# Optimization experiments

Hardware: AMD Instinct MI355X
Metric: run time of the kernel (lower is better)

The kernel has to match this reference:

```python
import jax, jax.numpy as jnp
import numpy as np

N = 6144      # nodes
NFEAT = 512
NHID = 256
NHEADS = 4
DHEAD = NHID // NHEADS  # 64
NEMBED = 128
NEG_INF = -9e15
LRELU_ALPHA = 0.2


def setup_inputs() -> dict:
    key = jax.random.key(0)
    k = jax.random.split(key, 8)
    x = jax.random.normal(k[0], (N, NFEAT), dtype=jnp.float32)
    adj = (jax.random.uniform(k[1], (N, N)) < 0.01).astype(jnp.int32)
    # per-head GAT params, packed over heads
    W = jax.random.normal(k[2], (NHEADS, NFEAT, DHEAD), dtype=jnp.float32) * 0.05
    a_src = jax.random.normal(k[3], (NHEADS, DHEAD), dtype=jnp.float32) * 0.05
    a_dst = jax.random.normal(k[4], (NHEADS, DHEAD), dtype=jnp.float32) * 0.05
    # output linear (init.normal_ std=0.05 per reset_parameters)
    lin_w = jax.random.normal(k[5], (NEMBED, NHID), dtype=jnp.float32) * 0.05
    lin_b = jnp.zeros((NEMBED,), dtype=jnp.float32)
    return {"x": x, "adj": adj, "W": W, "a_src": a_src, "a_dst": a_dst,
            "lin_w": lin_w, "lin_b": lin_b}


def _gat_forward(x, adj, W, a_src, a_dst, lin_w, lin_b):
    # Wh: [H, N, D]
    Wh = jnp.einsum('nf,hfd->hnd', x, W)
    # attention logits e_ij = leakyrelu(a_src.Wh_i + a_dst.Wh_j): [H, N, N]
    s = jnp.einsum('hnd,hd->hn', Wh, a_src)   # source term per node
    t = jnp.einsum('hnd,hd->hn', Wh, a_dst)   # target term per node
    e = s[:, :, None] + t[:, None, :]
    e = jax.nn.leaky_relu(e, negative_slope=LRELU_ALPHA)
    # mask by adjacency, softmax over neighbors
    e = jnp.where(adj[None, :, :] > 0, e, NEG_INF)
    attn = jax.nn.softmax(e, axis=-1)
    # aggregate and per-head ELU (concat=True GAT layer)
    h = jnp.einsum('hnm,hmd->hnd', attn, Wh)
    h = jax.nn.elu(h)
    # concat heads -> [N, NHID]
    h = jnp.transpose(h, (1, 0, 2)).reshape(N, NHID)
    # dropout is identity in eval mode; linear + ELU
    out = jax.nn.elu(h @ lin_w.T + lin_b)
    return out


def reference(x, adj, W, a_src, a_dst, lin_w, lin_b):
    return _gat_forward(x, adj, W, a_src, a_dst, lin_w, lin_b)
```

## Files before the change

kernel.cpp:

```cpp
#include <hip/hip_runtime.h>
#include <hip/hip_bf16.h>
#include <math.h>

#define N_NODES 6144
#define NFEAT 512
#define NHID 256
#define NHEADS 4
#define DHEAD 64
#define NEMBED 128
#define LRELU_ALPHA 0.2f
#define MAXC 256
#define ASTRIDE 20

static __device__ __forceinline__ unsigned short f2bf(float f) {
    unsigned u = __float_as_uint(f);
    unsigned r = (u + 0x7FFFu + ((u >> 16) & 1u)) >> 16;
    return (unsigned short)r;
}
static __device__ __forceinline__ float bfLo(unsigned u) { return __uint_as_float(u << 16); }
static __device__ __forceinline__ float bfHi(unsigned u) { return __uint_as_float(u & 0xffff0000u); }

__global__ __launch_bounds__(256) void gemm_scan(const float* __restrict__ x,
                                                 const float* __restrict__ W,
                                                 const float* __restrict__ a_src,
                                                 const float* __restrict__ a_dst,
                                                 const int* __restrict__ adj,
                                                 unsigned short* __restrict__ Whb,
                                                 float* __restrict__ s_arr,
                                                 float* __restrict__ t_arr,
                                                 int* __restrict__ cnt_g,
                                                 unsigned short* __restrict__ nbr_g) {
    __shared__ float As[64][ASTRIDE];
    __shared__ float Bs[16][64];
    __shared__ int scnt;
    const int tid = threadIdx.x;

    if (blockIdx.y < NHEADS) {
        const int tx = tid & 15;
        const int ty = tid >> 4;
        const int row0 = blockIdx.x * 64;
        const int h = blockIdx.y;
        const float* Bp = W + (size_t)h * NFEAT * DHEAD;

        float acc[4][4] = {};

        for (int k0 = 0; k0 < NFEAT; k0 += 16) {
            {
                const int r = tid >> 2, kq = tid & 3;
                const float4 v = *(const float4*)(x + (size_t)(row0 + r) * NFEAT + k0 + kq * 4);
                *(float4*)&As[r][kq * 4] = v;
            }
            {
                const int kk = tid >> 4, cq = tid & 15;
                const float4 v = *(const float4*)(Bp + (size_t)(k0 + kk) * DHEAD + cq * 4);
                *(float4*)&Bs[kk][cq * 4] = v;
            }
            __syncthreads();
#pragma unroll
            for (int kk = 0; kk < 16; kk++) {
                float a[4], b[4];
#pragma unroll
                for (int i = 0; i < 4; i++) a[i] = As[ty * 4 + i][kk];
#pragma unroll
                for (int j = 0; j < 4; j++) b[j] = Bs[kk][tx * 4 + j];
#pragma unroll
                for (int i = 0; i < 4; i++)
#pragma unroll
                    for (int j = 0; j < 4; j++) acc[i][j] += a[i] * b[j];
            }
            __syncthreads();
        }
#pragma unroll
        for (int i = 0; i < 4; i++) {
            const int row = row0 + ty * 4 + i;
            ushort4 w;
            w.x = f2bf(acc[i][0]);
            w.y = f2bf(acc[i][1]);
            w.z = f2bf(acc[i][2]);
            w.w = f2bf(acc[i][3]);
            *(ushort4*)(Whb + ((size_t)h * N_NODES + row) * DHEAD + tx * 4) = w;
        }
        float a4s[4], a4d[4];
#pragma unroll
        for (int j = 0; j < 4; j++) {
            a4s[j] = a_src[h * DHEAD + tx * 4 + j];
            a4d[j] = a_dst[h * DHEAD + tx * 4 + j];
        }
#pragma unroll
        for (int i = 0; i < 4; i++) {
            float ps = acc[i][0] * a4s[0] + acc[i][1] * a4s[1] +
                       acc[i][2] * a4s[2] + acc[i][3] * a4s[3];
            float pt = acc[i][0] * a4d[0] + acc[i][1] * a4d[1] +
                       acc[i][2] * a4d[2] + acc[i][3] * a4d[3];
#pragma unroll
            for (int off = 1; off < 16; off <<= 1) {
                ps += __shfl_xor(ps, off);
                pt += __shfl_xor(pt, off);
            }
            if (tx == 0) {
                const int row = row0 + ty * 4 + i;
                s_arr[h * N_NODES + row] = ps;
                t_arr[h * N_NODES + row] = pt;
            }
        }
    } else {
        const int r = (blockIdx.y - NHEADS) * gridDim.x + blockIdx.x;
        const int* arow = adj + (size_t)r * N_NODES;
        unsigned short* nrow = nbr_g + (size_t)r * MAXC;
        if (tid == 0) scnt = 0;
        __syncthreads();
#pragma unroll
        for (int it = 0; it < 6; ++it) {
            const int j0 = it * 1024 + tid * 4;
            const int4 v = *(const int4*)(arow + j0);
            const int n = (v.x != 0) + (v.y != 0) + (v.z != 0) + (v.w != 0);
            if (n) {
                int base = atomicAdd(&scnt, n);
                if (v.x) { if (base < MAXC) nrow[base] = (unsigned short)j0; ++base; }
                if (v.y) { if (base < MAXC) nrow[base] = (unsigned short)(j0 + 1); ++base; }
                if (v.z) { if (base < MAXC) nrow[base] = (unsigned short)(j0 + 2); ++base; }
                if (v.w) { if (base < MAXC) nrow[base] = (unsigned short)(j0 + 3); }
            }
        }
        __syncthreads();
        if (tid == 0) cnt_g[r] = scnt;
    }
}

__global__ __launch_bounds__(256) void attn_agg(const int* __restrict__ adj,
                                                const unsigned short* __restrict__ Whb,
                                                const float* __restrict__ s_arr,
                                                const float* __restrict__ t_arr,
                                                const int* __restrict__ cnt_g,
                                                const unsigned short* __restrict__ nbr_g,
                                                float* __restrict__ hcat) {
    __shared__ unsigned short nbr[MAXC];
    __shared__ float p_s[NHEADS][MAXC];
    const int i = blockIdx.x;
    const int tid = threadIdx.x;
    const int h = tid >> 6;
    const int lane = tid & 63;
    const int q = lane >> 4;
    const int dq = (lane & 15) * 4;
    const int c = cnt_g[i];
    const unsigned short* wp = Whb + (size_t)h * N_NODES * DHEAD;

    float b0[4] = {0.f, 0.f, 0.f, 0.f};
    float l = 1.0f;
    bool combine = true;

    if (c > 0 && c <= MAXC) {
        for (int k = tid; k < c; k += 256) nbr[k] = nbr_g[(size_t)i * MAXC + k];
        __syncthreads();

        const float s_h = s_arr[h * N_NODES + i];
        const float* tp = t_arr + (size_t)h * N_NODES;
        float m = -INFINITY;
        for (int k = lane; k < c; k += 64) {
            float e = s_h + tp[nbr[k]];
            e = e >= 0.0f ? e : LRELU_ALPHA * e;
            p_s[h][k] = e;
            m = fmaxf(m, e);
        }
#pragma unroll
        for (int off = 32; off > 0; off >>= 1) m = fmaxf(m, __shfl_xor(m, off));
        float ls = 0.0f;
        for (int k = lane; k < c; k += 64) {
            const float p = __expf(p_s[h][k] - m);
            p_s[h][k] = p;
            ls += p;
        }
#pragma unroll
        for (int off = 32; off > 0; off >>= 1) ls += __shfl_xor(ls, off);
        l = ls;

        float b1[4] = {0.f, 0.f, 0.f, 0.f};
        float b2[4] = {0.f, 0.f, 0.f, 0.f};
        float b3[4] = {0.f, 0.f, 0.f, 0.f};
        int k = 0;
        for (; k + 16 <= c; k += 16) {
            const int k0 = k + q, k1 = k + 4 + q, k2 = k + 8 + q, k3 = k + 12 + q;
            const int j0 = nbr[k0], j1 = nbr[k1], j2 = nbr[k2], j3 = nbr[k3];
            const float p0 = p_s[h][k0], p1 = p_s[h][k1];
            const float p2 = p_s[h][k2], p3 = p_s[h][k3];
            const uint2 w0 = *(const uint2*)(wp + (size_t)j0 * DHEAD + dq);
            const uint2 w1 = *(const uint2*)(wp + (size_t)j1 * DHEAD + dq);
            const uint2 w2 = *(const uint2*)(wp + (size_t)j2 * DHEAD + dq);
            const uint2 w3 = *(const uint2*)(wp + (size_t)j3 * DHEAD + dq);
            b0[0] += p0 * bfLo(w0.x); b0[1] += p0 * bfHi(w0.x);
            b0[2] += p0 * bfLo(w0.y); b0[3] += p0 * bfHi(w0.y);
            b1[0] += p1 * bfLo(w1.x); b1[1] += p1 * bfHi(w1.x);
            b1[2] += p1 * bfLo(w1.y); b1[3] += p1 * bfHi(w1.y);
            b2[0] += p2 * bfLo(w2.x); b2[1] += p2 * bfHi(w2.x);
            b2[2] += p2 * bfLo(w2.y); b2[3] += p2 * bfHi(w2.y);
            b3[0] += p3 * bfLo(w3.x); b3[1] += p3 * bfHi(w3.x);
            b3[2] += p3 * bfLo(w3.y); b3[3] += p3 * bfHi(w3.y);
        }
        for (; k < c; k += 4) {
            const int kk = k + q;
            const int j = (kk < c) ? nbr[kk] : nbr[k];
            const float p = (kk < c) ? p_s[h][kk] : 0.0f;
            const uint2 w = *(const uint2*)(wp + (size_t)j * DHEAD + dq);
            b0[0] += p * bfLo(w.x); b0[1] += p * bfHi(w.x);
            b0[2] += p * bfLo(w.y); b0[3] += p * bfHi(w.y);
        }
#pragma unroll
        for (int d = 0; d < 4; d++) b0[d] = (b0[d] + b1[d]) + (b2[d] + b3[d]);
    } else if (c == 0) {
        for (int j = q; j < N_NODES; j += 4) {
            const uint2 w = *(const uint2*)(wp + (size_t)j * DHEAD + dq);
            b0[0] += bfLo(w.x); b0[1] += bfHi(w.x);
            b0[2] += bfLo(w.y); b0[3] += bfHi(w.y);
        }
        l = (float)N_NODES;
    } else {
        combine = false;
        const int* arow = adj + (size_t)i * N_NODES;
        const float s_h = s_arr[h * N_NODES + i];
        const float* tp = t_arr + (size_t)h * N_NODES;
        float m = -INFINITY, ll = 0.0f;
        for (int j = 0; j < N_NODES; j++) {
            if (arow[j]) {
                float e = s_h + tp[j];
                e = e >= 0.0f ? e : LRELU_ALPHA * e;
                const float m_new = fmaxf(m, e);
                const float scale = __expf(m - m_new);
                const float p = __expf(e - m_new);
                ll = ll * scale + p;
                const uint2 w = *(const uint2*)(wp + (size_t)j * DHEAD + dq);
                b0[0] = b0[0] * scale + p * bfLo(w.x);
                b0[1] = b0[1] * scale + p * bfHi(w.x);
                b0[2] = b0[2] * scale + p * bfLo(w.y);
                b0[3] = b0[3] * scale + p * bfHi(w.y);
                m = m_new;
            }
        }
        l = ll;
    }

    if (combine) {
#pragma unroll
        for (int d = 0; d < 4; d++) {
            b0[d] += __shfl_xor(b0[d], 16);
            b0[d] += __shfl_xor(b0[d], 32);
        }
    }
    if (lane < 16) {
        float4 hv;
        float* pv = &hv.x;
#pragma unroll
        for (int d = 0; d < 4; d++) {
            float v = b0[d] / l;
            pv[d] = v > 0.0f ? v : expm1f(v);
        }
        *(float4*)(hcat + (size_t)i * NHID + h * DHEAD + dq) = hv;
    }
}

__global__ __launch_bounds__(256) void out_gemm(const float* __restrict__ hcat,
                                                const float* __restrict__ lin_w,
                                                const float* __restrict__ lin_b,
                                                float* __restrict__ out) {
    __shared__ float As[64][ASTRIDE * 4];
    __shared__ float Bs[16][64];
    const int tid = threadIdx.x;
    const int tx = tid & 15;
    const int ty = tid >> 4;
    const int row0 = blockIdx.x * 64;
    const int c0 = blockIdx.y * 64;

    float acc[4][4] = {};

    for (int k0 = 0; k0 < NHID; k0 += 16) {
        {
            const int r = tid >> 2, kq = tid & 3;
            const float4 v = *(const float4*)(hcat + (size_t)(row0 + r) * NHID + k0 + kq * 4);
            *(float4*)&As[r][kq * 4] = v;
        }
        {
            const int cc = tid & 63, kq = tid >> 6;
            const float4 v = *(const float4*)(lin_w + (size_t)(c0 + cc) * NHID + k0 + kq * 4);
            Bs[kq * 4 + 0][cc] = v.x;
            Bs[kq * 4 + 1][cc] = v.y;
            Bs[kq * 4 + 2][cc] = v.z;
            Bs[kq * 4 + 3][cc] = v.w;
        }
        __syncthreads();
#pragma unroll
        for (int kk = 0; kk < 16; kk++) {
            float a[4], b[4];
#pragma unroll
            for (int i = 0; i < 4; i++) a[i] = As[ty * 4 + i][kk];
#pragma unroll
            for (int j = 0; j < 4; j++) b[j] = Bs[kk][tx * 4 + j];
#pragma unroll
            for (int i = 0; i < 4; i++)
#pragma unroll
                for (int j = 0; j < 4; j++) acc[i][j] += a[i] * b[j];
        }
        __syncthreads();
    }
#pragma unroll
    for (int i = 0; i < 4; i++) {
        const int row = row0 + ty * 4 + i;
        float v[4];
#pragma unroll
        for (int j = 0; j < 4; j++) {
            const int col = c0 + tx * 4 + j;
            float val = acc[i][j] + lin_b[col];
            v[j] = val > 0.0f ? val : expm1f(val);
        }
        *(float4*)(out + (size_t)row * NEMBED + c0 + tx * 4) =
            make_float4(v[0], v[1], v[2], v[3]);
    }
}

extern "C" void kernel_launch(void* const* d_in, const int* in_sizes, int n_in,
                              void* d_out, int out_size, void* d_ws, size_t ws_size,
                              hipStream_t stream) {
    const float* x     = (const float*)d_in[0];
    const int*   adj   = (const int*)d_in[1];
    const float* W     = (const float*)d_in[2];
    const float* a_src = (const float*)d_in[3];
    const float* a_dst = (const float*)d_in[4];
    const float* lin_w = (const float*)d_in[5];
    const float* lin_b = (const float*)d_in[6];
    float* out = (float*)d_out;

    unsigned short* Whb = (unsigned short*)d_ws;
    float* s    = (float*)(Whb + (size_t)NHEADS * N_NODES * DHEAD);
    float* t    = s + (size_t)NHEADS * N_NODES;
    float* hcat = t + (size_t)NHEADS * N_NODES;
    int* cnt_g  = (int*)(hcat + (size_t)N_NODES * NHID);
    unsigned short* nbr_g = (unsigned short*)(cnt_g + N_NODES);

    gemm_scan<<<dim3(96, NHEADS + 64), 256, 0, stream>>>(
        x, W, a_src, a_dst, adj, Whb, s, t, cnt_g, nbr_g);
    attn_agg<<<N_NODES, 256, 0, stream>>>(adj, Whb, s, t, cnt_g, nbr_g, hcat);
    out_gemm<<<dim3(N_NODES / 64, NEMBED / 64), 256, 0, stream>>>(hcat, lin_w, lin_b, out);
}
```

Measured before the change: 278.3 us.

## Compute Wh projection with split-bf16 MFMA instead of scalar FP32 FMA

Replaces the scalar FP32 register-tiled GEMM for x·W with bf16 MFMA 16x16x32 instructions. Each fp32 operand is split into high and low bf16 parts and three MFMAs are issued (hi*hi, hi*lo, lo*hi) to keep accuracy close to fp32. B is stored transposed in shared memory with an XOR swizzle to avoid bank conflicts. The cost is extra conversion work and three times the MFMA count, traded against the much higher matrix-core throughput, and the result is slightly less accurate than true fp32.

```diff
diff --git a/kernel.cpp b/kernel.cpp
--- a/kernel.cpp
+++ b/kernel.cpp
@@ -12,10 +12,20 @@
 #define MAXC 256
 #define ASTRIDE 20
 
+typedef __attribute__((ext_vector_type(8))) __bf16 bfrag;
+typedef __attribute__((ext_vector_type(4))) float f32x4;
+
 static __device__ __forceinline__ unsigned short f2bf(float f) {
     unsigned u = __float_as_uint(f);
     unsigned r = (u + 0x7FFFu + ((u >> 16) & 1u)) >> 16;
     return (unsigned short)r;
+}
+static __device__ __forceinline__ float bf2f(unsigned short b) {
+    return __uint_as_float((unsigned)b << 16);
+}
+static __device__ __forceinline__ void split1(float v, unsigned short& h, unsigned short& l) {
+    h = f2bf(v);
+    l = f2bf(v - bf2f(h));
 }
 static __device__ __forceinline__ float bfLo(unsigned u) { return __uint_as_float(u << 16); }
 static __device__ __forceinline__ float bfHi(unsigned u) { return __uint_as_float(u & 0xffff0000u); }
@@ -30,83 +40,99 @@
                                                  float* __restrict__ t_arr,
                                                  int* __restrict__ cnt_g,
                                                  unsigned short* __restrict__ nbr_g) {
-    __shared__ float As[64][ASTRIDE];
-    __shared__ float Bs[16][64];
+    __shared__ unsigned short Ah[64][32];
+    __shared__ unsigned short Al[64][32];
+    __shared__ unsigned short Bh[64][32];
+    __shared__ unsigned short Bl[64][32];
     __shared__ int scnt;
     const int tid = threadIdx.x;
 
     if (blockIdx.y < NHEADS) {
-        const int tx = tid & 15;
-        const int ty = tid >> 4;
+        const int h = blockIdx.y;
         const int row0 = blockIdx.x * 64;
-        const int h = blockIdx.y;
+        const int w = tid >> 6;
+        const int lane = tid & 63;
+        const int g = lane >> 4;
+        const int r = lane & 15;
         const float* Bp = W + (size_t)h * NFEAT * DHEAD;
 
-        float acc[4][4] = {};
-
-        for (int k0 = 0; k0 < NFEAT; k0 += 16) {
+        f32x4 acc[4] = {};
+
+        const int ar = tid >> 2, akq = (tid & 3) * 8;
+        const int bkk = tid >> 3, bnq = tid & 7;
+        const int bks = bkk ^ ((bnq & 3) << 3);
+
+        for (int k0 = 0; k0 < NFEAT; k0 += 32) {
+            const float4 av0 = *(const float4*)(x + (size_t)(row0 + ar) * NFEAT + k0 + akq);
+            const float4 av1 = *(const float4*)(x + (size_t)(row0 + ar) * NFEAT + k0 + akq + 4);
+            ushort4 h0, l0, h1, l1;
+            split1(av0.x, h0.x, l0.x); split1(av0.y, h0.y, l0.y);
+            split1(av0.z, h0.z, l0.z); split1(av0.w, h0.w, l0.w);
+            split1(av1.x, h1.x, l1.x); split1(av1.y, h1.y, l1.y);
+            split1(av1.z, h1.z, l1.z); split1(av1.w, h1.w, l1.w);
+            *(ushort4*)&Ah[ar][akq]     = h0;
+            *(ushort4*)&Ah[ar][akq + 4] = h1;
+            *(ushort4*)&Al[ar][akq]     = l0;
+            *(ushort4*)&Al[ar][akq + 4] = l1;
+            const float4 bv0 = *(const float4*)(Bp + (size_t)(k0 + bkk) * DHEAD + bnq * 8);
+            const float4 bv1 = *(const float4*)(Bp + (size_t)(k0 + bkk) * DHEAD + bnq * 8 + 4);
             {
-                const int r = tid >> 2, kq = tid & 3;
-                const float4 v = *(const float4*)(x + (size_t)(row0 + r) * NFEAT + k0 + kq * 4);
-                *(float4*)&As[r][kq * 4] = v;
-            }
-            {
-                const int kk = tid >> 4, cq = tid & 15;
-                const float4 v = *(const float4*)(Bp + (size_t)(k0 + kk) * DHEAD + cq * 4);
-                *(float4*)&Bs[kk][cq * 4] = v;
+                unsigned short hh, ll;
+                split1(bv0.x, hh, ll); Bh[bnq * 8 + 0][bks] = hh; Bl[bnq * 8 + 0][bks] = ll;
+                split1(bv0.y, hh, ll); Bh[bnq * 8 + 1][bks] = hh; Bl[bnq * 8 + 1][bks] = ll;
+                split1(bv0.z, hh, ll); Bh[bnq * 8 + 2][bks] = hh; Bl[bnq * 8 + 2][bks] = ll;
+                split1(bv0.w, hh, ll); Bh[bnq * 8 + 3][bks] = hh; Bl[bnq * 8 + 3][bks] = ll;
+                split1(bv1.x, hh, ll); Bh[bnq * 8 + 4][bks] = hh; Bl[bnq * 8 + 4][bks] = ll;
+                split1(bv1.y, hh, ll); Bh[bnq * 8 + 5][bks] = hh; Bl[bnq * 8 + 5][bks] = ll;
+                split1(bv1.z, hh, ll); Bh[bnq * 8 + 6][bks] = hh; Bl[bnq * 8 + 6][bks] = ll;
+                split1(bv1.w, hh, ll); Bh[bnq * 8 + 7][bks] = hh; Bl[bnq * 8 + 7][bks] = ll;
             }
             __syncthreads();
-#pragma unroll
-            for (int kk = 0; kk < 16; kk++) {
-                float a[4], b[4];
-#pragma unroll
-                for (int i = 0; i < 4; i++) a[i] = As[ty * 4 + i][kk];
-#pragma unroll
-                for (int j = 0; j < 4; j++) b[j] = Bs[kk][tx * 4 + j];
-#pragma unroll
-                for (int i = 0; i < 4; i++)
-#pragma unroll
-                    for (int j = 0; j < 4; j++) acc[i][j] += a[i] * b[j];
+            const int arow = w * 16 + r;
+            const bfrag ah = *(const bfrag*)&Ah[arow][g * 8];
+            const bfrag al = *(const bfrag*)&Al[arow][g * 8];
+#pragma unroll
+            for (int nt = 0; nt < 4; nt++) {
+                const int blk = (g ^ ((2 * nt + (r >> 3)) & 3)) * 8;
+                const bfrag bh = *(const bfrag*)&Bh[nt * 16 + r][blk];
+                const bfrag bl = *(const bfrag*)&Bl[nt * 16 + r][blk];
+                acc[nt] = __builtin_amdgcn_mfma_f32_16x16x32_bf16(ah, bh, acc[nt], 0, 0, 0);
+                acc[nt] = __builtin_amdgcn_mfma_f32_16x16x32_bf16(ah, bl, acc[nt], 0, 0, 0);
+                acc[nt] = __builtin_amdgcn_mfma_f32_16x16x32_bf16(al, bh, acc[nt], 0, 0, 0);
             }
             __syncthreads();
         }
-#pragma unroll
-        for (int i = 0; i < 4; i++) {
-            const int row = row0 + ty * 4 + i;
-            ushort4 w;
-            w.x = f2bf(acc[i][0]);
-            w.y = f2bf(acc[i][1]);
-            w.z = f2bf(acc[i][2]);
-            w.w = f2bf(acc[i][3]);
-            *(ushort4*)(Whb + ((size_t)h * N_NODES + row) * DHEAD + tx * 4) = w;
-        }
-        float a4s[4], a4d[4];
-#pragma unroll
-        for (int j = 0; j < 4; j++) {
-            a4s[j] = a_src[h * DHEAD + tx * 4 + j];
-            a4d[j] = a_dst[h * DHEAD + tx * 4 + j];
-        }
-#pragma unroll
-        for (int i = 0; i < 4; i++) {
-            float ps = acc[i][0] * a4s[0] + acc[i][1] * a4s[1] +
-                       acc[i][2] * a4s[2] + acc[i][3] * a4s[3];
-            float pt = acc[i][0] * a4d[0] + acc[i][1] * a4d[1] +
-                       acc[i][2] * a4d[2] + acc[i][3] * a4d[3];
+        float asv[4], adv[4];
+#pragma unroll
+        for (int nt = 0; nt < 4; nt++) {
+            asv[nt] = a_src[h * DHEAD + nt * 16 + r];
+            adv[nt] = a_dst[h * DHEAD + nt * 16 + r];
+        }
+        const int mbase = row0 + w * 16 + 4 * g;
+#pragma unroll
+        for (int q = 0; q < 4; q++) {
+            const int m = mbase + q;
+#pragma unroll
+            for (int nt = 0; nt < 4; nt++)
+                Whb[((size_t)h * N_NODES + m) * DHEAD + nt * 16 + r] = f2bf(acc[nt][q]);
+            float ps = acc[0][q] * asv[0] + acc[1][q] * asv[1] +
+                       acc[2][q] * asv[2] + acc[3][q] * asv[3];
+            float pt = acc[0][q] * adv[0] + acc[1][q] * adv[1] +
+                       acc[2][q] * adv[2] + acc[3][q] * adv[3];
 #pragma unroll
             for (int off = 1; off < 16; off <<= 1) {
                 ps += __shfl_xor(ps, off);
                 pt += __shfl_xor(pt, off);
             }
-            if (tx == 0) {
-                const int row = row0 + ty * 4 + i;
-                s_arr[h * N_NODES + row] = ps;
-                t_arr[h * N_NODES + row] = pt;
+            if (r == 0) {
+                s_arr[h * N_NODES + m] = ps;
+                t_arr[h * N_NODES + m] = pt;
             }
         }
     } else {
-        const int r = (blockIdx.y - NHEADS) * gridDim.x + blockIdx.x;
-        const int* arow = adj + (size_t)r * N_NODES;
-        unsigned short* nrow = nbr_g + (size_t)r * MAXC;
+        const int rr = (blockIdx.y - NHEADS) * gridDim.x + blockIdx.x;
+        const int* arow = adj + (size_t)rr * N_NODES;
+        unsigned short* nrow = nbr_g + (size_t)rr * MAXC;
         if (tid == 0) scnt = 0;
         __syncthreads();
 #pragma unroll
@@ -123,7 +149,7 @@
             }
         }
         __syncthreads();
-        if (tid == 0) cnt_g[r] = scnt;
+        if (tid == 0) cnt_g[rr] = scnt;
     }
 }
 
```

New measurement: 275.7 us. No clear change (-0.9%).
